# Performance work log

Measured on AMD Instinct MI355X. Metric: run time of the kernel, lower is better.

Reference implementation:

```python
import jax, jax.numpy as jnp
import numpy as np

MARGIN = 0.2
EPS = 1e-6  # torch.pairwise_distance adds eps to the difference before the norm


def setup_inputs() -> dict:
    key = jax.random.key(0)
    k1, k2, k3 = jax.random.split(key, 3)
    B, D = 8192, 128
    emb1 = jax.random.normal(k1, (B, D), dtype=jnp.float32)
    emb2 = jax.random.normal(k2, (B, D), dtype=jnp.float32)
    target = jax.random.randint(k3, (B,), 0, 2, dtype=jnp.int64)
    return {"emb1": emb1, "emb2": emb2, "target": target}


def reference(emb1, emb2, target):
    B, D = emb1.shape
    # torch.pairwise_distance(a, b) = ||a - b + EPS||_2; expand the square:
    # |a-b+eps|^2 = |a|^2 + |b|^2 - 2 a.b + 2*eps*(sum(a)-sum(b)) + D*eps^2
    sq = (
        jnp.sum(emb1 * emb1, axis=-1)[:, None]
        + jnp.sum(emb2 * emb2, axis=-1)[None, :]
        - 2.0 * (emb1 @ emb2.T)
        + 2.0 * EPS * (jnp.sum(emb1, axis=-1)[:, None] - jnp.sum(emb2, axis=-1)[None, :])
        + D * EPS * EPS
    )
    dist = jnp.sqrt(jnp.maximum(sq, 0.0))  # [B, B]: dist[i, j] = ||emb1[i] - emb2[j] + eps||

    pos = target == 1
    neg = target == 0
    # hardest positive: max over columns j with target[j]==1; hardest negative: min over target[j]==0
    pos_max = jnp.max(jnp.where(pos[None, :], dist, -jnp.inf), axis=1)  # [B]
    neg_min = jnp.min(jnp.where(neg[None, :], dist, jnp.inf), axis=1)   # [B]
    per_anchor = jnp.maximum(pos_max - neg_min + MARGIN, 0.0)
    anchor_w = pos.astype(dist.dtype)
    # mean over anchors (rows i with target[i]==1)
    return jnp.sum(per_anchor * anchor_w) / jnp.sum(anchor_w)
```

## Files before the change

kernel.cpp:

```cpp
#include <hip/hip_runtime.h>
#include <hip/hip_bf16.h>
#include <math.h>


#define DDIM   128
#define SPLITS 8
#define MARGIN 0.2f
#define EPS    1e-6f
#define SENT   1e30f

#define CHUNK_PITCH 1056
#define WAVE_SPAN   (8 * CHUNK_PITCH)
#define TILE_BYTES  (4 * WAVE_SPAN)

typedef unsigned short ushort_t;
typedef __attribute__((ext_vector_type(8))) short short8;
typedef __attribute__((ext_vector_type(4))) float f32x4;

__device__ __forceinline__ ushort_t f2bf(float f) {
    unsigned int u = __float_as_uint(f);
    u = (u + 0x7FFFu + ((u >> 16) & 1u)) >> 16;
    return (ushort_t)u;
}

__device__ __forceinline__ void g2lds16(const ushort_t* g, void* lds) {
    __builtin_amdgcn_global_load_lds(
        (const __attribute__((address_space(1))) unsigned int*)g,
        (__attribute__((address_space(3))) unsigned int*)lds,
        16, 0, 0);
}

__global__ void prep_kernel(const float* __restrict__ e1, const float* __restrict__ e2,
                            const int* __restrict__ target,
                            ushort_t* __restrict__ e1b, ushort_t* __restrict__ e2b,
                            float* __restrict__ rowterm,
                            float* __restrict__ cpos, float* __restrict__ cneg,
                            float* __restrict__ redsum, int* __restrict__ ticket, int B) {
    if (blockIdx.x == 0 && threadIdx.x == 0) {
        redsum[0] = 0.f; redsum[1] = 0.f; *ticket = 0;
    }
    int w    = (blockIdx.x * blockDim.x + threadIdx.x) >> 6;
    int lane = threadIdx.x & 63;
    if (w >= 2 * B) return;
    bool first = (w < B);
    int r = first ? w : w - B;
    const float* src = (first ? e1 : e2) + (size_t)r * DDIM;
    float2 v = *(const float2*)(src + lane * 2);
    ushort_t* dst = (first ? e1b : e2b) + (size_t)r * DDIM;
    ushort2 o; o.x = f2bf(v.x); o.y = f2bf(v.y);
    *(ushort2*)(dst + lane * 2) = o;
    float s = v.x + v.y;
    float n = v.x * v.x + v.y * v.y;
    #pragma unroll
    for (int off = 32; off > 0; off >>= 1) {
        s += __shfl_down(s, off, 64);
        n += __shfl_down(n, off, 64);
    }
    if (lane == 0) {
        if (first) {
            rowterm[r] = n + 2.f * EPS * s + (float)DDIM * EPS * EPS;
        } else {
            float ct = n - 2.f * EPS * s;
            int tg = target[r];
            cpos[r] = (tg == 1) ? ct : -SENT;
            cneg[r] = (tg == 0) ? ct :  SENT;
        }
    }
}

__device__ __forceinline__ void stage_tile_dma(const ushort_t* __restrict__ gRow0,
                                               unsigned char* __restrict__ lds,
                                               int w, int l) {
    const ushort_t* g = gRow0 + (size_t)(w * 32) * DDIM + l * 8;
    unsigned char* lp = lds + w * WAVE_SPAN;
    #pragma unroll
    for (int it = 0; it < 8; ++it)
        g2lds16(g + it * 512, lp + it * CHUNK_PITCH);
}

__global__ __launch_bounds__(256, 2)
void tile_kernel(const ushort_t* __restrict__ e1b, const ushort_t* __restrict__ e2b,
                 const float* __restrict__ cpos, const float* __restrict__ cneg,
                 float* __restrict__ pmp, float* __restrict__ nmp, int B) {
    __shared__ __align__(16) unsigned char As[TILE_BYTES];
    __shared__ __align__(16) unsigned char Bs[TILE_BYTES];

    const int tid = threadIdx.x;
    const int w   = tid >> 6;
    const int l   = tid & 63;
    const int lq  = l >> 4;
    const int lm  = l & 15;
    const int row0 = blockIdx.x * 128;
    const int colSpan = B / SPLITS;
    const int col0 = blockIdx.y * colSpan;
    const int nTiles = colSpan / 128;

    const int wr = (w >> 1) * 64;
    const int wc = (w & 1) * 64;

    const unsigned char* aLane = As + ((wr >> 2) + (lm >> 2)) * CHUNK_PITCH
                                    + (lm & 3) * 256 + lq * 16;
    const unsigned char* bLane = Bs + ((wc >> 2) + (lm >> 2)) * CHUNK_PITCH
                                    + (lm & 3) * 256 + lq * 16;

    stage_tile_dma(e1b + (size_t)row0 * DDIM, As, w, l);
    stage_tile_dma(e2b + (size_t)col0 * DDIM, Bs, w, l);
    __syncthreads();

    short8 afr[4][4];
    #pragma unroll
    for (int i = 0; i < 4; ++i)
        #pragma unroll
        for (int k4 = 0; k4 < 4; ++k4)
            afr[i][k4] = *(const short8*)(aLane + i * (4 * CHUNK_PITCH) + k4 * 64);

    float pm[4][4], nm[4][4];
    #pragma unroll
    for (int i = 0; i < 4; ++i)
        #pragma unroll
        for (int r = 0; r < 4; ++r) { pm[i][r] = -SENT; nm[i][r] = SENT; }

    for (int t = 0; t < nTiles; ++t) {
        f32x4 acc[4][4];
        #pragma unroll
        for (int i = 0; i < 4; ++i)
            #pragma unroll
            for (int j = 0; j < 4; ++j)
                acc[i][j] = (f32x4){0.f, 0.f, 0.f, 0.f};

        #pragma unroll
        for (int kk = 0; kk < DDIM; kk += 32) {
            const int k4 = kk >> 5;
            const int ko = kk * 2;
            short8 bf[4];
            #pragma unroll
            for (int j = 0; j < 4; ++j)
                bf[j] = *(const short8*)(bLane + j * (4 * CHUNK_PITCH) + ko);
            #pragma unroll
            for (int i = 0; i < 4; ++i)
                #pragma unroll
                for (int j = 0; j < 4; ++j)
                    acc[i][j] = __builtin_amdgcn_mfma_f32_16x16x32_bf16(
                                    afr[i][k4], bf[j], acc[i][j], 0, 0, 0);
        }

        #pragma unroll
        for (int j = 0; j < 4; ++j) {
            int col = col0 + t * 128 + wc + j * 16 + lm;
            float cp = cpos[col];
            float cn = cneg[col];
            #pragma unroll
            for (int i = 0; i < 4; ++i)
                #pragma unroll
                for (int r = 0; r < 4; ++r) {
                    float d = acc[i][j][r];
                    pm[i][r] = fmaxf(pm[i][r], fmaf(-2.f, d, cp));
                    nm[i][r] = fminf(nm[i][r], fmaf(-2.f, d, cn));
                }
        }

        if (t + 1 < nTiles) {
            __syncthreads();
            stage_tile_dma(e2b + (size_t)(col0 + (t + 1) * 128) * DDIM, Bs, w, l);
            __syncthreads();
        }
    }

    #pragma unroll
    for (int m = 1; m < 16; m <<= 1) {
        #pragma unroll
        for (int i = 0; i < 4; ++i)
            #pragma unroll
            for (int r = 0; r < 4; ++r) {
                pm[i][r] = fmaxf(pm[i][r], __shfl_xor(pm[i][r], m, 64));
                nm[i][r] = fminf(nm[i][r], __shfl_xor(nm[i][r], m, 64));
            }
    }

    __syncthreads();
    float* smP = (float*)As;
    float* smN = smP + 128;
    if ((w & 1) == 1 && lm == 0) {
        #pragma unroll
        for (int i = 0; i < 4; ++i)
            #pragma unroll
            for (int r = 0; r < 4; ++r) {
                int lr = wr + i * 16 + lq * 4 + r;
                smP[lr] = pm[i][r];
                smN[lr] = nm[i][r];
            }
    }
    __syncthreads();
    if ((w & 1) == 0 && lm == 0) {
        #pragma unroll
        for (int i = 0; i < 4; ++i)
            #pragma unroll
            for (int r = 0; r < 4; ++r) {
                int lr  = wr + i * 16 + lq * 4 + r;
                int row = row0 + lr;
                pmp[(size_t)blockIdx.y * B + row] = fmaxf(pm[i][r], smP[lr]);
                nmp[(size_t)blockIdx.y * B + row] = fminf(nm[i][r], smN[lr]);
            }
    }
}

__global__ void reduce_kernel(const float* __restrict__ pmp, const float* __restrict__ nmp,
                              const float* __restrict__ rowterm, const int* __restrict__ target,
                              float* __restrict__ redsum, int* __restrict__ ticket,
                              float* __restrict__ out, int B) {
    int row = blockIdx.x * blockDim.x + threadIdx.x;
    float s = 0.f, c = 0.f;
    {
        float pmv = -SENT, nmv = SENT;
        #pragma unroll
        for (int sp = 0; sp < SPLITS; ++sp) {
            pmv = fmaxf(pmv, pmp[(size_t)sp * B + row]);
            nmv = fminf(nmv, nmp[(size_t)sp * B + row]);
        }
        float rt = rowterm[row];
        float dp = sqrtf(fmaxf(rt + pmv, 0.f));
        float dn = sqrtf(fmaxf(rt + nmv, 0.f));
        if (target[row] == 1) {
            s = fmaxf(dp - dn + MARGIN, 0.f);
            c = 1.f;
        }
    }
    #pragma unroll
    for (int off = 32; off > 0; off >>= 1) {
        s += __shfl_down(s, off, 64);
        c += __shfl_down(c, off, 64);
    }
    __shared__ float ls[4], lc[4];
    int wv = threadIdx.x >> 6, ln = threadIdx.x & 63;
    if (ln == 0) { ls[wv] = s; lc[wv] = c; }
    __syncthreads();
    if (threadIdx.x == 0) {
        float ss = ls[0] + ls[1] + ls[2] + ls[3];
        float cc = lc[0] + lc[1] + lc[2] + lc[3];
        atomicAdd(&redsum[0], ss);
        atomicAdd(&redsum[1], cc);
        __threadfence();
        int done = atomicAdd(ticket, 1);
        if (done == (int)gridDim.x - 1) {
            __threadfence();
            float fs = __hip_atomic_load(&redsum[0], __ATOMIC_RELAXED, __HIP_MEMORY_SCOPE_AGENT);
            float fc = __hip_atomic_load(&redsum[1], __ATOMIC_RELAXED, __HIP_MEMORY_SCOPE_AGENT);
            out[0] = fs / fc;
        }
    }
}

extern "C" void kernel_launch(void* const* d_in, const int* in_sizes, int n_in,
                              void* d_out, int out_size, void* d_ws, size_t ws_size,
                              hipStream_t stream) {
    const float* e1     = (const float*)d_in[0];
    const float* e2     = (const float*)d_in[1];
    const int*   target = (const int*)d_in[2];
    float* out = (float*)d_out;
    const int B = in_sizes[2];

    char* p = (char*)d_ws;
    ushort_t* e1b  = (ushort_t*)p;   p += (size_t)B * DDIM * 2;
    ushort_t* e2b  = (ushort_t*)p;   p += (size_t)B * DDIM * 2;
    float* rowterm = (float*)p;      p += (size_t)B * 4;
    float* cpos    = (float*)p;      p += (size_t)B * 4;
    float* cneg    = (float*)p;      p += (size_t)B * 4;
    float* pmp     = (float*)p;      p += (size_t)SPLITS * B * 4;
    float* nmp     = (float*)p;      p += (size_t)SPLITS * B * 4;
    float* redsum  = (float*)p;      p += 2 * 4;
    int*   ticket  = (int*)p;

    {
        int blocks = (2 * B + 3) / 4;
        prep_kernel<<<blocks, 256, 0, stream>>>(e1, e2, target, e1b, e2b,
                                                rowterm, cpos, cneg, redsum, ticket, B);
    }
    {
        dim3 grid(B / 128, SPLITS);
        tile_kernel<<<grid, 256, 0, stream>>>(e1b, e2b, cpos, cneg, pmp, nmp, B);
    }
    reduce_kernel<<<32, 256, 0, stream>>>(pmp, nmp, rowterm, target,
                                          redsum, ticket, out, B);
}
```

Measured before the change: 90.55 us.

## Double-buffer B tiles in LDS and load A fragments directly from global

Replaces the single B tile buffer with two LDS buffers, so the DMA for tile t+1 is issued before computing on tile t, and drops one of the two barriers per iteration. The A operand fragments are now read straight from global memory into registers rather than staged through LDS, which frees the A buffer's space for the second B buffer. This is meant to hide global-to-LDS load latency behind the MFMA work. The risk is that relying on a single barrier per iteration may not fully cover completion of the async copy before the next read, and the uncoalesced global A loads may cost more.

```diff
diff --git a/kernel.cpp b/kernel.cpp
--- a/kernel.cpp
+++ b/kernel.cpp
@@ -68,22 +68,12 @@
     }
 }
 
-__device__ __forceinline__ void stage_tile_dma(const ushort_t* __restrict__ gRow0,
-                                               unsigned char* __restrict__ lds,
-                                               int w, int l) {
-    const ushort_t* g = gRow0 + (size_t)(w * 32) * DDIM + l * 8;
-    unsigned char* lp = lds + w * WAVE_SPAN;
-    #pragma unroll
-    for (int it = 0; it < 8; ++it)
-        g2lds16(g + it * 512, lp + it * CHUNK_PITCH);
-}
-
 __global__ __launch_bounds__(256, 2)
 void tile_kernel(const ushort_t* __restrict__ e1b, const ushort_t* __restrict__ e2b,
                  const float* __restrict__ cpos, const float* __restrict__ cneg,
                  float* __restrict__ pmp, float* __restrict__ nmp, int B) {
-    __shared__ __align__(16) unsigned char As[TILE_BYTES];
-    __shared__ __align__(16) unsigned char Bs[TILE_BYTES];
+    __shared__ __align__(16) unsigned char Bs[2][TILE_BYTES];
+    __shared__ float smP[128], smN[128];
 
     const int tid = threadIdx.x;
     const int w   = tid >> 6;
@@ -98,29 +88,41 @@
     const int wr = (w >> 1) * 64;
     const int wc = (w & 1) * 64;
 
-    const unsigned char* aLane = As + ((wr >> 2) + (lm >> 2)) * CHUNK_PITCH
-                                    + (lm & 3) * 256 + lq * 16;
-    const unsigned char* bLane = Bs + ((wc >> 2) + (lm >> 2)) * CHUNK_PITCH
-                                    + (lm & 3) * 256 + lq * 16;
-
-    stage_tile_dma(e1b + (size_t)row0 * DDIM, As, w, l);
-    stage_tile_dma(e2b + (size_t)col0 * DDIM, Bs, w, l);
-    __syncthreads();
+    auto stageB = [&](int t, int buf) {
+        const ushort_t* g = e2b + (size_t)(col0 + t * 128 + w * 32) * DDIM + l * 8;
+        unsigned char* lp = Bs[buf] + w * WAVE_SPAN;
+        #pragma unroll
+        for (int it = 0; it < 8; ++it)
+            g2lds16(g + it * 512, lp + it * CHUNK_PITCH);
+    };
+
+    stageB(0, 0);
 
     short8 afr[4][4];
+    {
+        const ushort_t* aG = e1b + (size_t)(row0 + wr + lm) * DDIM + lq * 8;
+        #pragma unroll
+        for (int i = 0; i < 4; ++i)
+            #pragma unroll
+            for (int k4 = 0; k4 < 4; ++k4)
+                afr[i][k4] = *(const short8*)(aG + i * 16 * DDIM + k4 * 32);
+    }
+
+    const int bOff = ((wc >> 2) + (lm >> 2)) * CHUNK_PITCH + (lm & 3) * 256 + lq * 16;
+
+    float pm[4][4], nm[4][4];
     #pragma unroll
     for (int i = 0; i < 4; ++i)
         #pragma unroll
-        for (int k4 = 0; k4 < 4; ++k4)
-            afr[i][k4] = *(const short8*)(aLane + i * (4 * CHUNK_PITCH) + k4 * 64);
-
-    float pm[4][4], nm[4][4];
-    #pragma unroll
-    for (int i = 0; i < 4; ++i)
-        #pragma unroll
         for (int r = 0; r < 4; ++r) { pm[i][r] = -SENT; nm[i][r] = SENT; }
 
+    __syncthreads();
+
     for (int t = 0; t < nTiles; ++t) {
+        if (t + 1 < nTiles) stageB(t + 1, (t + 1) & 1);
+
+        const unsigned char* bLane = Bs[t & 1] + bOff;
+
         f32x4 acc[4][4];
         #pragma unroll
         for (int i = 0; i < 4; ++i)
@@ -159,11 +161,8 @@
                 }
         }
 
-        if (t + 1 < nTiles) {
+        if (t + 1 < nTiles)
             __syncthreads();
-            stage_tile_dma(e2b + (size_t)(col0 + (t + 1) * 128) * DDIM, Bs, w, l);
-            __syncthreads();
-        }
     }
 
     #pragma unroll
@@ -178,8 +177,6 @@
     }
 
     __syncthreads();
-    float* smP = (float*)As;
-    float* smN = smP + 128;
     if ((w & 1) == 1 && lm == 0) {
         #pragma unroll
         for (int i = 0; i < 4; ++i)
```

New measurement: 92.09 us. About the same (+1.7%).
